# Performance work log

Hardware: AMD Instinct MI355X
Metric: run time of the kernel (lower is better)

## Reference

```python
import jax, jax.numpy as jnp
import numpy as np

B, N, D, H = 16, 576, 768, 8
HD = D // H
SCALE = HD ** -0.5
EPS = 1e-5  # torch LayerNorm default


def _ln(x, g, b):
    mu = jnp.mean(x, axis=-1, keepdims=True)
    var = jnp.mean(jnp.square(x - mu), axis=-1, keepdims=True)
    return (x - mu) * jax.lax.rsqrt(var + EPS) * g + b


def setup_inputs() -> dict:
    key = jax.random.key(0)
    ks = jax.random.split(key, 20)
    s = D ** -0.5
    inp = {
        "x1": jax.random.normal(ks[0], (B, N, D), jnp.float32),
        "x2": jax.random.normal(ks[1], (B, N, D), jnp.float32),
        # projection weights stored [in, out]
        "Wq": jax.random.normal(ks[2], (D, D), jnp.float32) * s,
        "bq": jnp.zeros((D,), jnp.float32),
        "Wk": jax.random.normal(ks[3], (D, D), jnp.float32) * s,
        "bk": jnp.zeros((D,), jnp.float32),
        "Wv": jax.random.normal(ks[4], (D, D), jnp.float32) * s,
        "bv": jnp.zeros((D,), jnp.float32),
        "Wo": jax.random.normal(ks[5], (D, D), jnp.float32) * s,
        "bo": jnp.zeros((D,), jnp.float32),
        "g1": jnp.ones((D,), jnp.float32),
        "be1": jnp.zeros((D,), jnp.float32),
        "g2": jnp.ones((D,), jnp.float32),
        "be2": jnp.zeros((D,), jnp.float32),
        "W1": jax.random.normal(ks[6], (D, 4 * D), jnp.float32) * s,
        "bf1": jnp.zeros((4 * D,), jnp.float32),
        "W2": jax.random.normal(ks[7], (4 * D, D), jnp.float32) * (4 * D) ** -0.5,
        "bf2": jnp.zeros((D,), jnp.float32),
    }
    return inp


def reference(x1, x2, Wq, bq, Wk, bk, Wv, bv, Wo, bo, g1, be1, g2, be2, W1, bf1, W2, bf2):
    def heads(x, W, b):
        # [B,N,D] -> [B,H,N,HD]
        return (x @ W + b).reshape(B, N, H, HD).transpose(0, 2, 1, 3)

    def block(xq, xkv):
        q = heads(xq, Wq, bq)
        k = heads(xkv, Wk, bk)
        v = heads(xkv, Wv, bv)
        attn = jax.nn.softmax(jnp.einsum('bhqd,bhkd->bhqk', q, k) * SCALE, axis=-1)
        o = jnp.einsum('bhqk,bhkd->bqhd', attn, v).reshape(B, N, D)
        o = o @ Wo + bo
        h = _ln(xq + o, g1, be1)
        f = jax.nn.gelu(h @ W1 + bf1, approximate=False) @ W2 + bf2
        return _ln(h + f, g2, be2), attn

    out1, a1 = block(x1, x2)
    out2, a2 = block(x2, x1)
    attn_map = (a1 + a2.transpose(0, 1, 3, 2)) * 0.5
    return out1, out2, attn_map
```

## Files before the change

### kernel.cpp

```cpp
#include <hip/hip_runtime.h>
#include <cstdint>
#include <cstddef>

#define B_   16
#define N_   576
#define D_   768
#define H_   8
#define HD_  96
#define DF_  3072
#define R_   (B_*N_)
#define SCALE_F 0.10206207261596575f

typedef __bf16 bf16;
typedef __attribute__((ext_vector_type(8))) __bf16 bf16x8;
typedef __attribute__((ext_vector_type(4))) __bf16 bf16x4;
typedef __attribute__((ext_vector_type(4))) float  f32x4;

__device__ __forceinline__ void gld_lds16(const void* g, void* l) {
  __builtin_amdgcn_global_load_lds((const __attribute__((address_space(1))) void*)g,
                                   (__attribute__((address_space(3))) void*)l,
                                   16, 0, 0);
}
__device__ __forceinline__ void nt_f32(float* p, float v) { __builtin_nontemporal_store(v, p); }
__device__ __forceinline__ float gelu_f(float v) {
  float u = 0.7978845608028654f * v * (1.0f + 0.044715f*v*v);
  float e = __expf(2.0f*u);
  float th = 1.0f - 2.0f/(e + 1.0f);
  return 0.5f*v*(1.0f + th);
}

__global__ void cast_f32_bf16_k(const float* __restrict__ x, bf16* __restrict__ y, int n4) {
  int i = blockIdx.x*256 + threadIdx.x;
  if (i >= n4) return;
  f32x4 v = ((const f32x4*)x)[i];
  union { bf16 h[4]; unsigned long long q; } u;
  u.h[0] = (bf16)v[0]; u.h[1] = (bf16)v[1]; u.h[2] = (bf16)v[2]; u.h[3] = (bf16)v[3];
  ((unsigned long long*)y)[i] = u.q;
}

__global__ void transpose_cast_k(const float* __restrict__ W, bf16* __restrict__ WT,
                                 int rows, int cols) {
  __shared__ float tile[32][33];
  int cb = blockIdx.x*32, rb = blockIdx.y*32;
  int tx = threadIdx.x, ty = threadIdx.y;
  #pragma unroll
  for (int i=0;i<32;i+=8)
    tile[ty+i][tx] = W[(size_t)(rb+ty+i)*cols + cb+tx];
  __syncthreads();
  #pragma unroll
  for (int i=0;i<32;i+=8)
    WT[(size_t)(cb+ty+i)*rows + rb+tx] = (bf16)tile[tx][ty+i];
}

__global__ void concat_bias_k(const float* a, const float* b, const float* c, float* o) {
  int i = blockIdx.x*256 + threadIdx.x;
  if (i < 768) o[i] = a[i];
  else if (i < 1536) o[i] = b[i-768];
  else if (i < 2304) o[i] = c[i-1536];
}

template<int EPI, int SWZ>
__global__ __launch_bounds__(512, 2) void gemm256_k(
    const bf16* __restrict__ A, const bf16* __restrict__ Bt,
    const float* __restrict__ bias,
    bf16* __restrict__ outB, bf16* __restrict__ outK, bf16* __restrict__ outVT,
    int Nn, int K, int nct)
{
  __shared__ __align__(16) char lds[65536];
  const int t = threadIdx.x;
  const int lane = t & 63, w = t >> 6, g = lane >> 4, r = lane & 15;
  const int wr = w >> 2, wc = w & 3;

  const int cpx = gridDim.x >> 3;
  const int xcd = blockIdx.x & 7, loc = blockIdx.x >> 3;
  int rt, ct;
  if (SWZ) {
    const int nrt_x = cpx / nct;
    ct = loc / nrt_x;
    rt = xcd * nrt_x + (loc - ct*nrt_x);
  } else {
    const int wg = xcd*cpx + loc;
    rt = wg / nct; ct = wg - rt*nct;
  }
  const size_t a0 = (size_t)rt*256, b0 = (size_t)ct*256;

  f32x4 acc[8][4];
  #pragma unroll
  for (int m=0;m<8;++m)
    #pragma unroll
    for (int n=0;n<4;++n) acc[m][n] = (f32x4){0.f,0.f,0.f,0.f};

  const int rbase = ((t>>6)<<4) + (t&15);
  const int kbase = ((t>>4)&3)*8;
  const bf16* Ab = A  + (a0 + rbase)*(size_t)K + kbase;
  const bf16* Bb = Bt + (b0 + rbase)*(size_t)K + kbase;
  const size_t rstep = (size_t)128*K;
  char* Al = lds + t*16;
  char* Bl = lds + 32768 + t*16;

#define STAGE256(tt, cc) do { \
    const size_t ko_ = (size_t)(tt)*32; \
    gld_lds16(Ab + ko_,         Al + (cc)*16384); \
    gld_lds16(Ab + rstep + ko_, Al + (cc)*16384 + 8192); \
    gld_lds16(Bb + ko_,         Bl + (cc)*16384); \
    gld_lds16(Bb + rstep + ko_, Bl + (cc)*16384 + 8192); \
  } while (0)

  const int NT = K >> 5;
  STAGE256(0, 0);
  for (int tt = 0; tt < NT; ++tt) {
    const int c = tt & 1;
    if (tt + 1 < NT) {
      STAGE256(tt + 1, c ^ 1);
      asm volatile("s_waitcnt vmcnt(4)" ::: "memory");
    } else {
      asm volatile("s_waitcnt vmcnt(0)" ::: "memory");
    }
    __builtin_amdgcn_sched_barrier(0);
    __builtin_amdgcn_s_barrier();
    __builtin_amdgcn_sched_barrier(0);

    const char* Ard = lds + c*16384 + (wr<<13) + lane*16;
    const char* Brd = lds + 32768 + c*16384 + (wc<<12) + lane*16;
    bf16x8 bfr[4], af[4];
    #pragma unroll
    for (int n=0;n<4;++n) bfr[n] = *(const bf16x8*)(Brd + n*1024);
    #pragma unroll
    for (int m=0;m<4;++m) af[m]  = *(const bf16x8*)(Ard + m*1024);
    __builtin_amdgcn_s_setprio(1);
    #pragma unroll
    for (int m=0;m<4;++m)
      #pragma unroll
      for (int n=0;n<4;++n)
        acc[m][n] = __builtin_amdgcn_mfma_f32_16x16x32_bf16(af[m], bfr[n], acc[m][n], 0, 0, 0);
    __builtin_amdgcn_s_setprio(0);
    #pragma unroll
    for (int m=0;m<4;++m) af[m] = *(const bf16x8*)(Ard + (4+m)*1024);
    __builtin_amdgcn_s_setprio(1);
    #pragma unroll
    for (int m=0;m<4;++m)
      #pragma unroll
      for (int n=0;n<4;++n)
        acc[4+m][n] = __builtin_amdgcn_mfma_f32_16x16x32_bf16(af[m], bfr[n], acc[4+m][n], 0, 0, 0);
    __builtin_amdgcn_s_setprio(0);
    __builtin_amdgcn_sched_barrier(0);
    __builtin_amdgcn_s_barrier();
    __builtin_amdgcn_sched_barrier(0);
  }
#undef STAGE256

  const int rowb = rt*256;
  const int colb = ct*256;
  bf16* lds16p = (bf16*)lds;
  const int g4 = g*4;
  const bool vtile = (EPI == 4) && (ct >= 6);

  #pragma unroll
  for (int ph = 0; ph < 2; ++ph) {
    __builtin_amdgcn_s_barrier();
    #pragma unroll
    for (int n = 0; n < 4; ++n) {
      const int col = wc*64 + n*16 + r;
      const float bc = bias[colb + col];
      #pragma unroll
      for (int m = 0; m < 4; ++m) {
        #pragma unroll
        for (int j = 0; j < 4; ++j) {
          float v = acc[ph*4+m][n][j] + bc;
          if (EPI == 3) v = gelu_f(v);
          const int rowin = m*16 + g4 + j;
          if (vtile) {
            lds16p[col*128 + wr*64 + (rowin ^ ((col&7)<<3))] = (bf16)v;
          } else {
            const int rowL = wr*64 + rowin;
            const int chs = ((col>>3) ^ ((rowL>>2)&7));
            lds16p[rowL*256 + (chs<<3) + (col&7)] = (bf16)v;
          }
        }
      }
    }
    __builtin_amdgcn_s_barrier();
    if (vtile) {
      #pragma unroll
      for (int i = 0; i < 8; ++i) {
        const int cid = i*512 + t;
        const int col = cid >> 4, chunk = cid & 15, run = chunk >> 3, k = chunk & 7;
        bf16x8 val = *(const bf16x8*)&lds16p[col*128 + run*64 + ((k ^ (col&7))<<3)];
        const int rowg = rowb + run*128 + ph*64 + k*8;
        const int s  = rowg >= R_;
        const int rr = rowg - s*R_;
        const int bb = rr / N_, nn = rr - bb*N_;
        bf16* p = outVT + (size_t)s*R_*D_ + ((size_t)bb*D_ + (ct-6)*256 + col)*N_ + nn;
        *(bf16x8*)p = val;
      }
    } else {
      #pragma unroll
      for (int i = 0; i < 8; ++i) {
        const int cid = i*512 + t;
        const int rl = cid >> 5, ch = cid & 31;
        bf16x8 val = *(const bf16x8*)&lds16p[rl*256 + ((ch ^ ((rl>>2)&7))<<3)];
        const int rowg = rowb + (rl>>6)*128 + ph*64 + (rl&63);
        const int c0 = colb + ch*8;
        if (EPI == 0 || EPI == 3) {
          *(bf16x8*)(outB + (size_t)rowg*Nn + c0) = val;
        } else {
          const int s  = rowg >= R_;
          const int rr = rowg - s*R_;
          const int bb = rr / N_, nn = rr - bb*N_;
          const size_t so = (size_t)s*R_*D_;
          bf16* p;
          if (c0 < 768) {
            const int hh = c0/96, dd = c0 - hh*96;
            p = outB + so + ((size_t)(bb*H_+hh)*N_ + nn)*HD_ + dd;
          } else {
            const int c1 = c0 - 768;
            const int hh = c1/96, dd = c1 - hh*96;
            p = outK + so + ((size_t)(bb*H_+hh)*N_ + nn)*HD_ + dd;
          }
          *(bf16x8*)p = val;
        }
      }
    }
  }
}


__global__ __launch_bounds__(256, 2) void attn_stats_k(
    const bf16* __restrict__ Q, const bf16* __restrict__ Kb,
    const bf16* __restrict__ VT, bf16* __restrict__ obuf,
    float* __restrict__ mrow, float* __restrict__ rrow)
{
  __shared__ __align__(16) char plds[2*18432 + 512];
  float* smax = (float*)(plds + 36864);
  float* ssum = smax + 64;
  const int t = threadIdx.x, w = t>>6, lane = t&63, g = lane>>4, r = lane&15;
  const int wq = w>>1, wc = w&1;
  const int h = blockIdx.x & 7, ii = blockIdx.x >> 3;
  const int b = ii/18, qt = ii - b*18, bh = b*8 + h;
  const int q0 = qt*32 + wq*16, c0 = wc*288, row4 = g*4;

  f32x4 s[18];
  #pragma unroll
  for (int n=0;n<18;++n) s[n] = (f32x4){0.f,0.f,0.f,0.f};
  bf16x8 aq[3];
  const bf16* qrow = Q + ((size_t)(b*H_+h)*N_ + q0 + r)*HD_;
  #pragma unroll
  for (int kk=0;kk<3;++kk) aq[kk] = *(const bf16x8*)(qrow + kk*32 + g*8);
  const bf16* kbase = Kb + ((size_t)(b*H_+h)*N_ + c0 + r)*HD_ + g*8;
  #pragma unroll
  for (int n=0;n<18;++n) {
    const bf16* kr = kbase + (size_t)(n*16)*HD_;
    bf16x8 b0 = *(const bf16x8*)(kr);
    bf16x8 b1 = *(const bf16x8*)(kr + 32);
    bf16x8 b2 = *(const bf16x8*)(kr + 64);
    __builtin_amdgcn_s_setprio(1);
    s[n] = __builtin_amdgcn_mfma_f32_16x16x32_bf16(aq[0], b0, s[n], 0, 0, 0);
    s[n] = __builtin_amdgcn_mfma_f32_16x16x32_bf16(aq[1], b1, s[n], 0, 0, 0);
    s[n] = __builtin_amdgcn_mfma_f32_16x16x32_bf16(aq[2], b2, s[n], 0, 0, 0);
    __builtin_amdgcn_s_setprio(0);
  }

  float mx[4], sum[4], rinv[4];
  #pragma unroll
  for (int j=0;j<4;++j) {
    float m = -1e30f;
    #pragma unroll
    for (int n=0;n<18;++n) m = fmaxf(m, s[n][j]);
    #pragma unroll
    for (int d=1; d<16; d<<=1) m = fmaxf(m, __shfl_xor(m, d));
    mx[j] = m;
  }
  if ((lane&15)==0) {
    #pragma unroll
    for (int j=0;j<4;++j) smax[(wq*2+wc)*16 + row4+j] = mx[j];
  }
  __syncthreads();
  #pragma unroll
  for (int j=0;j<4;++j) {
    mx[j] = fmaxf(mx[j], smax[(wq*2+(wc^1))*16 + row4+j]);
    sum[j] = 0.f;
  }
  #pragma unroll
  for (int n=0;n<18;++n)
    #pragma unroll
    for (int j=0;j<4;++j) {
      float p = __expf((s[n][j] - mx[j]) * SCALE_F);
      s[n][j] = p; sum[j] += p;
    }
  #pragma unroll
  for (int j=0;j<4;++j) {
    #pragma unroll
    for (int d=1; d<16; d<<=1) sum[j] += __shfl_xor(sum[j], d);
  }
  if ((lane&15)==0) {
    #pragma unroll
    for (int j=0;j<4;++j) ssum[(wq*2+wc)*16 + row4+j] = sum[j];
  }
  __syncthreads();
  #pragma unroll
  for (int j=0;j<4;++j)
    rinv[j] = 1.0f / (sum[j] + ssum[(wq*2+(wc^1))*16 + row4+j]);

  if (wc==0 && (lane&15)==0) {
    const size_t sb = (size_t)bh*N_ + q0 + row4;
    #pragma unroll
    for (int j=0;j<4;++j) { mrow[sb+j] = mx[j]; rrow[sb+j] = rinv[j]; }
  }

  char* pw = plds + wq*18432;
  #pragma unroll
  for (int n=0;n<18;++n)
    #pragma unroll
    for (int j=0;j<4;++j) {
      int kc = c0 + n*16 + r, row = row4 + j;
      *(bf16*)(pw + ((kc>>3)<<8) + (row<<4) + ((kc&7)<<1)) = (bf16)(s[n][j]*rinv[j]);
    }
  __syncthreads();

  f32x4 oa[3];
  #pragma unroll
  for (int n=0;n<3;++n) oa[n] = (f32x4){0.f,0.f,0.f,0.f};
  const bf16* vtb = VT + ((size_t)b*D_ + h*HD_ + wc*48 + r)*N_ + g*8;
  for (int kt=0; kt<18; ++kt) {
    bf16x8 pa = *(const bf16x8*)(pw + kt*1024 + lane*16);
    bf16x8 v0 = *(const bf16x8*)(vtb + kt*32);
    bf16x8 v1 = *(const bf16x8*)(vtb + (size_t)16*N_ + kt*32);
    bf16x8 v2 = *(const bf16x8*)(vtb + (size_t)32*N_ + kt*32);
    __builtin_amdgcn_s_setprio(1);
    oa[0] = __builtin_amdgcn_mfma_f32_16x16x32_bf16(pa, v0, oa[0], 0, 0, 0);
    oa[1] = __builtin_amdgcn_mfma_f32_16x16x32_bf16(pa, v1, oa[1], 0, 0, 0);
    oa[2] = __builtin_amdgcn_mfma_f32_16x16x32_bf16(pa, v2, oa[2], 0, 0, 0);
    __builtin_amdgcn_s_setprio(0);
  }
  #pragma unroll
  for (int n=0;n<3;++n)
    #pragma unroll
    for (int j=0;j<4;++j)
      obuf[((size_t)b*N_ + q0+row4+j)*D_ + h*HD_ + wc*48 + n*16 + r] = (bf16)oa[n][j];
}

__global__ __launch_bounds__(256, 2) void attn_map_k(
    const bf16* __restrict__ Q1, const bf16* __restrict__ K2,
    const bf16* __restrict__ VT2, const bf16* __restrict__ K1,
    const bf16* __restrict__ Q2, const float* __restrict__ mrow,
    const float* __restrict__ rrow, float* __restrict__ attn_out,
    bf16* __restrict__ obuf)
{
  __shared__ __align__(16) char plds[2*18432 + 512];
  float* smax = (float*)(plds + 36864);
  float* ssum = smax + 64;
  const int t = threadIdx.x, w = t>>6, lane = t&63, g = lane>>4, r = lane&15;
  const int wq = w>>1, wc = w&1;
  const int h = blockIdx.x & 7, ii = blockIdx.x >> 3;
  const int b = ii/18, qt = ii - b*18, bh = b*8 + h;
  const int q0 = qt*32 + wq*16, c0 = wc*288, row4 = g*4;

  f32x4 s[18];
  #pragma unroll
  for (int n=0;n<18;++n) s[n] = (f32x4){0.f,0.f,0.f,0.f};
  bf16x8 aq[3];
  const bf16* qrow = Q1 + ((size_t)(b*H_+h)*N_ + q0 + r)*HD_;
  #pragma unroll
  for (int kk=0;kk<3;++kk) aq[kk] = *(const bf16x8*)(qrow + kk*32 + g*8);
  const bf16* kbase = K2 + ((size_t)(b*H_+h)*N_ + c0 + r)*HD_ + g*8;
  #pragma unroll
  for (int n=0;n<18;++n) {
    const bf16* kr = kbase + (size_t)(n*16)*HD_;
    bf16x8 b0 = *(const bf16x8*)(kr);
    bf16x8 b1 = *(const bf16x8*)(kr + 32);
    bf16x8 b2 = *(const bf16x8*)(kr + 64);
    __builtin_amdgcn_s_setprio(1);
    s[n] = __builtin_amdgcn_mfma_f32_16x16x32_bf16(aq[0], b0, s[n], 0, 0, 0);
    s[n] = __builtin_amdgcn_mfma_f32_16x16x32_bf16(aq[1], b1, s[n], 0, 0, 0);
    s[n] = __builtin_amdgcn_mfma_f32_16x16x32_bf16(aq[2], b2, s[n], 0, 0, 0);
    __builtin_amdgcn_s_setprio(0);
  }

  float mx[4], sum[4], rinv[4];
  #pragma unroll
  for (int j=0;j<4;++j) {
    float m = -1e30f;
    #pragma unroll
    for (int n=0;n<18;++n) m = fmaxf(m, s[n][j]);
    #pragma unroll
    for (int d=1; d<16; d<<=1) m = fmaxf(m, __shfl_xor(m, d));
    mx[j] = m;
  }
  if ((lane&15)==0) {
    #pragma unroll
    for (int j=0;j<4;++j) smax[(wq*2+wc)*16 + row4+j] = mx[j];
  }
  __syncthreads();
  #pragma unroll
  for (int j=0;j<4;++j) {
    mx[j] = fmaxf(mx[j], smax[(wq*2+(wc^1))*16 + row4+j]);
    sum[j] = 0.f;
  }
  #pragma unroll
  for (int n=0;n<18;++n)
    #pragma unroll
    for (int j=0;j<4;++j) {
      float p = __expf((s[n][j] - mx[j]) * SCALE_F);
      s[n][j] = p; sum[j] += p;
    }
  #pragma unroll
  for (int j=0;j<4;++j) {
    #pragma unroll
    for (int d=1; d<16; d<<=1) sum[j] += __shfl_xor(sum[j], d);
  }
  if ((lane&15)==0) {
    #pragma unroll
    for (int j=0;j<4;++j) ssum[(wq*2+wc)*16 + row4+j] = sum[j];
  }
  __syncthreads();
  #pragma unroll
  for (int j=0;j<4;++j)
    rinv[j] = 1.0f / (sum[j] + ssum[(wq*2+(wc^1))*16 + row4+j]);

  char* pw = plds + wq*18432;
  #pragma unroll
  for (int n=0;n<18;++n)
    #pragma unroll
    for (int j=0;j<4;++j) {
      int kc = c0 + n*16 + r, row = row4 + j;
      *(bf16*)(pw + ((kc>>3)<<8) + (row<<4) + ((kc&7)<<1)) = (bf16)(s[n][j]*rinv[j]);
    }
  __syncthreads();

  f32x4 oa[3];
  #pragma unroll
  for (int n=0;n<3;++n) oa[n] = (f32x4){0.f,0.f,0.f,0.f};
  const bf16* vtb = VT2 + ((size_t)b*D_ + h*HD_ + wc*48 + r)*N_ + g*8;
  for (int kt=0; kt<18; ++kt) {
    bf16x8 pa = *(const bf16x8*)(pw + kt*1024 + lane*16);
    bf16x8 v0 = *(const bf16x8*)(vtb + kt*32);
    bf16x8 v1 = *(const bf16x8*)(vtb + (size_t)16*N_ + kt*32);
    bf16x8 v2 = *(const bf16x8*)(vtb + (size_t)32*N_ + kt*32);
    __builtin_amdgcn_s_setprio(1);
    oa[0] = __builtin_amdgcn_mfma_f32_16x16x32_bf16(pa, v0, oa[0], 0, 0, 0);
    oa[1] = __builtin_amdgcn_mfma_f32_16x16x32_bf16(pa, v1, oa[1], 0, 0, 0);
    oa[2] = __builtin_amdgcn_mfma_f32_16x16x32_bf16(pa, v2, oa[2], 0, 0, 0);
    __builtin_amdgcn_s_setprio(0);
  }
  #pragma unroll
  for (int n=0;n<3;++n)
    #pragma unroll
    for (int j=0;j<4;++j)
      obuf[((size_t)b*N_ + q0+row4+j)*D_ + h*HD_ + wc*48 + n*16 + r] = (bf16)oa[n][j];

  #pragma unroll
  for (int n=0;n<18;++n) s[n] = (f32x4){0.f,0.f,0.f,0.f};
  bf16x8 ak[3];
  const bf16* k1row = K1 + ((size_t)(b*H_+h)*N_ + q0 + r)*HD_;
  #pragma unroll
  for (int kk=0;kk<3;++kk) ak[kk] = *(const bf16x8*)(k1row + kk*32 + g*8);
  const bf16* q2b = Q2 + ((size_t)(b*H_+h)*N_ + c0 + r)*HD_ + g*8;
  #pragma unroll
  for (int n=0;n<18;++n) {
    const bf16* qr2 = q2b + (size_t)(n*16)*HD_;
    bf16x8 b0 = *(const bf16x8*)(qr2);
    bf16x8 b1 = *(const bf16x8*)(qr2 + 32);
    bf16x8 b2 = *(const bf16x8*)(qr2 + 64);
    __builtin_amdgcn_s_setprio(1);
    s[n] = __builtin_amdgcn_mfma_f32_16x16x32_bf16(ak[0], b0, s[n], 0, 0, 0);
    s[n] = __builtin_amdgcn_mfma_f32_16x16x32_bf16(ak[1], b1, s[n], 0, 0, 0);
    s[n] = __builtin_amdgcn_mfma_f32_16x16x32_bf16(ak[2], b2, s[n], 0, 0, 0);
    __builtin_amdgcn_s_setprio(0);
  }

  const float* mb = mrow + (size_t)bh*N_;
  const float* rb = rrow + (size_t)bh*N_;
  float* aout = attn_out + (size_t)bh*N_*N_;
  #pragma unroll
  for (int n=0;n<18;++n) {
    const int kc = c0 + n*16 + r;
    const float m2v = mb[kc];
    const float rv  = rb[kc];
    #pragma unroll
    for (int j=0;j<4;++j) {
      const int row = row4 + j;
      float p1 = (float)(*(const bf16*)(pw + ((kc>>3)<<8) + (row<<4) + ((kc&7)<<1)));
      float a2t = __expf((s[n][j] - m2v) * SCALE_F) * rv;
      nt_f32(aout + (size_t)(q0 + row)*N_ + kc, 0.5f*(p1 + a2t));
    }
  }
}

template<int MODE>
__global__ __launch_bounds__(256) void ln_k(
    const float* __restrict__ xf1, const float* __restrict__ xf2,
    const bf16* __restrict__ xb, const bf16* __restrict__ y,
    const float* __restrict__ gamma, const float* __restrict__ beta,
    bf16* __restrict__ out16, float* __restrict__ out32)
{
  const int w = threadIdx.x>>6, lane = threadIdx.x&63;
  const size_t row = (size_t)blockIdx.x*4 + w;
  float v[12]; float s = 0.f, s2 = 0.f;
  const bf16* yr = y + row*D_;
  #pragma unroll
  for (int i=0;i<3;++i) {
    int c = i*256 + lane*4;
    bf16x4 bb = *(const bf16x4*)(yr + c);
    float xr4[4];
    if (MODE == 0) {
      const float* xr = (row < R_) ? (xf1 + row*D_) : (xf2 + (row-R_)*D_);
      f32x4 a = *(const f32x4*)(xr + c);
      #pragma unroll
      for (int q=0;q<4;++q) xr4[q] = a[q];
    } else {
      bf16x4 a = *(const bf16x4*)(xb + row*D_ + c);
      #pragma unroll
      for (int q=0;q<4;++q) xr4[q] = (float)a[q];
    }
    #pragma unroll
    for (int q=0;q<4;++q) {
      float tq = xr4[q] + (float)bb[q];
      v[i*4+q] = tq; s += tq; s2 += tq*tq;
    }
  }
  #pragma unroll
  for (int d=1; d<64; d<<=1) { s += __shfl_xor(s, d); s2 += __shfl_xor(s2, d); }
  const float mean = s*(1.f/D_);
  const float var  = s2*(1.f/D_) - mean*mean;
  const float rstd = rsqrtf(var + 1e-5f);
  #pragma unroll
  for (int i=0;i<3;++i) {
    int c = i*256 + lane*4;
    f32x4 gm = *(const f32x4*)(gamma + c);
    f32x4 bt = *(const f32x4*)(beta  + c);
    float o[4];
    #pragma unroll
    for (int q=0;q<4;++q) o[q] = (v[i*4+q]-mean)*rstd*gm[q] + bt[q];
    if (MODE == 0) {
      union { bf16 h[4]; unsigned long long q64; } u;
      u.h[0]=(bf16)o[0]; u.h[1]=(bf16)o[1]; u.h[2]=(bf16)o[2]; u.h[3]=(bf16)o[3];
      *(unsigned long long*)(out16 + row*D_ + c) = u.q64;
    } else {
      f32x4 ov = {o[0], o[1], o[2], o[3]};
      __builtin_nontemporal_store(ov, (f32x4*)(out32 + row*D_ + c));
    }
  }
}

extern "C" void kernel_launch(void* const* d_in, const int* in_sizes, int n_in,
                              void* d_out, int out_size, void* d_ws, size_t ws_size,
                              hipStream_t stream)
{
  const float* x1  = (const float*)d_in[0];
  const float* x2  = (const float*)d_in[1];
  const float* Wq  = (const float*)d_in[2];  const float* bq  = (const float*)d_in[3];
  const float* Wk  = (const float*)d_in[4];  const float* bk  = (const float*)d_in[5];
  const float* Wv  = (const float*)d_in[6];  const float* bv  = (const float*)d_in[7];
  const float* Wo  = (const float*)d_in[8];  const float* bo  = (const float*)d_in[9];
  const float* g1  = (const float*)d_in[10]; const float* be1 = (const float*)d_in[11];
  const float* g2  = (const float*)d_in[12]; const float* be2 = (const float*)d_in[13];
  const float* W1  = (const float*)d_in[14]; const float* bf1 = (const float*)d_in[15];
  const float* W2  = (const float*)d_in[16]; const float* bf2 = (const float*)d_in[17];

  float* outLN = (float*)d_out;
  float* attn  = outLN + (size_t)2*R_*D_;

  char* ws = (char*)d_ws;
  size_t off = 0;
  auto alloc = [&](size_t bytes) -> void* {
    void* p = ws + off;
    off += (bytes + 255) & ~(size_t)255;
    return p;
  };
  const size_t RD2 = (size_t)R_*D_*2;
  size_t span1 = off;
  bf16* xb  = (bf16*)alloc(2*RD2);
  bf16* Qb  = (bf16*)alloc(2*RD2);
  bf16* Kb  = (bf16*)alloc(2*RD2);
  bf16* VTb = (bf16*)alloc(2*RD2);
  bf16* G   = (bf16*)(ws + span1);
  bf16* wqkvT = (bf16*)alloc((size_t)2304*D_*2);
  float* bqkv = (float*)alloc(2304*4);
  bf16* woT   = (bf16*)alloc((size_t)D_*D_*2);
  bf16* w1T   = (bf16*)alloc((size_t)D_*DF_*2);
  bf16* w2T   = (bf16*)alloc((size_t)DF_*D_*2);
  bf16* obuf  = (bf16*)alloc(2*RD2);
  bf16* oprojB= (bf16*)alloc(2*RD2);
  bf16* h16   = (bf16*)alloc(2*RD2);
  bf16* f16   = (bf16*)alloc(2*RD2);
  float* m2r  = (float*)alloc((size_t)B_*H_*N_*4);
  float* r2r  = (float*)alloc((size_t)B_*H_*N_*4);
  (void)ws_size; (void)in_sizes; (void)n_in; (void)out_size;

  const int n4 = R_*D_/4;
  cast_f32_bf16_k<<<n4/256, 256, 0, stream>>>(x1, xb, n4);
  cast_f32_bf16_k<<<n4/256, 256, 0, stream>>>(x2, xb + (size_t)R_*D_, n4);

  dim3 tb(32,8);
  transpose_cast_k<<<dim3(24,24), tb, 0, stream>>>(Wq, wqkvT,             D_, D_);
  transpose_cast_k<<<dim3(24,24), tb, 0, stream>>>(Wk, wqkvT + 768*D_,    D_, D_);
  transpose_cast_k<<<dim3(24,24), tb, 0, stream>>>(Wv, wqkvT + 1536*D_,   D_, D_);
  transpose_cast_k<<<dim3(24,24), tb, 0, stream>>>(Wo, woT, D_, D_);
  transpose_cast_k<<<dim3(96,24), tb, 0, stream>>>(W1, w1T, D_, DF_);
  transpose_cast_k<<<dim3(24,96), tb, 0, stream>>>(W2, w2T, DF_, D_);
  concat_bias_k<<<9, 256, 0, stream>>>(bq, bk, bv, bqkv);

  gemm256_k<4,1><<<648, 512, 0, stream>>>(xb, wqkvT, bqkv, Qb, Kb, VTb, 2304, 768, 9);

  const size_t SD = (size_t)R_*D_;
  attn_stats_k<<<2304, 256, 0, stream>>>(Qb + SD, Kb, VTb, obuf + SD, m2r, r2r);
  attn_map_k  <<<2304, 256, 0, stream>>>(Qb, Kb + SD, VTb + SD, Kb, Qb + SD, m2r, r2r, attn, obuf);

  gemm256_k<0,1><<<216, 512, 0, stream>>>(obuf, woT, bo, oprojB, nullptr, nullptr, 768, 768, 3);
  ln_k<0><<<2*R_/4, 256, 0, stream>>>(x1, x2, nullptr, oprojB, g1, be1, h16, nullptr);
  gemm256_k<3,1><<<864, 512, 0, stream>>>(h16, w1T, bf1, G, nullptr, nullptr, 3072, 768, 12);
  gemm256_k<0,0><<<216, 512, 0, stream>>>(G, w2T, bf2, f16, nullptr, nullptr, 768, 3072, 3);
  ln_k<1><<<2*R_/4, 256, 0, stream>>>(nullptr, nullptr, h16, f16, g2, be2, nullptr, outLN);
}
```

Before: 728.9 us.

## Deepen GEMM LDS pipeline with 64-wide K tiles and interleaved staged loads

Restructures the 256x256 bf16 GEMM main loop to use 64-wide K tiles split into two 32-wide halves. The loop is double-buffered across 128KB of LDS. Global-to-LDS loads for the next A and B halves are spread between the four MFMA quarter-phases, each fenced by barriers, so memory traffic overlaps compute at finer granularity. The larger LDS footprint likely allows only one workgroup per CU, and the extra barriers add synchronization cost.

```diff
diff --git a/kernel.cpp b/kernel.cpp
--- a/kernel.cpp
+++ b/kernel.cpp
@@ -66,10 +66,11 @@
     bf16* __restrict__ outB, bf16* __restrict__ outK, bf16* __restrict__ outVT,
     int Nn, int K, int nct)
 {
-  __shared__ __align__(16) char lds[65536];
+  __shared__ __align__(16) char lds[131072];
   const int t = threadIdx.x;
   const int lane = t & 63, w = t >> 6, g = lane >> 4, r = lane & 15;
   const int wr = w >> 2, wc = w & 3;
+  const int lane16 = lane*16;
 
   const int cpx = gridDim.x >> 3;
   const int xcd = blockIdx.x & 7, loc = blockIdx.x >> 3;
@@ -90,64 +91,70 @@
     #pragma unroll
     for (int n=0;n<4;++n) acc[m][n] = (f32x4){0.f,0.f,0.f,0.f};
 
-  const int rbase = ((t>>6)<<4) + (t&15);
-  const int kbase = ((t>>4)&3)*8;
-  const bf16* Ab = A  + (a0 + rbase)*(size_t)K + kbase;
-  const bf16* Bb = Bt + (b0 + rbase)*(size_t)K + kbase;
-  const size_t rstep = (size_t)128*K;
-  char* Al = lds + t*16;
-  char* Bl = lds + 32768 + t*16;
-
-#define STAGE256(tt, cc) do { \
-    const size_t ko_ = (size_t)(tt)*32; \
-    gld_lds16(Ab + ko_,         Al + (cc)*16384); \
-    gld_lds16(Ab + rstep + ko_, Al + (cc)*16384 + 8192); \
-    gld_lds16(Bb + ko_,         Bl + (cc)*16384); \
-    gld_lds16(Bb + rstep + ko_, Bl + (cc)*16384 + 8192); \
-  } while (0)
-
-  const int NT = K >> 5;
-  STAGE256(0, 0);
-  for (int tt = 0; tt < NT; ++tt) {
-    const int c = tt & 1;
-    if (tt + 1 < NT) {
-      STAGE256(tt + 1, c ^ 1);
-      asm volatile("s_waitcnt vmcnt(4)" ::: "memory");
-    } else {
-      asm volatile("s_waitcnt vmcnt(0)" ::: "memory");
-    }
-    __builtin_amdgcn_sched_barrier(0);
-    __builtin_amdgcn_s_barrier();
-    __builtin_amdgcn_sched_barrier(0);
-
-    const char* Ard = lds + c*16384 + (wr<<13) + lane*16;
-    const char* Brd = lds + 32768 + c*16384 + (wc<<12) + lane*16;
-    bf16x8 bfr[4], af[4];
-    #pragma unroll
-    for (int n=0;n<4;++n) bfr[n] = *(const bf16x8*)(Brd + n*1024);
-    #pragma unroll
-    for (int m=0;m<4;++m) af[m]  = *(const bf16x8*)(Ard + m*1024);
-    __builtin_amdgcn_s_setprio(1);
-    #pragma unroll
-    for (int m=0;m<4;++m)
-      #pragma unroll
-      for (int n=0;n<4;++n)
-        acc[m][n] = __builtin_amdgcn_mfma_f32_16x16x32_bf16(af[m], bfr[n], acc[m][n], 0, 0, 0);
-    __builtin_amdgcn_s_setprio(0);
-    #pragma unroll
-    for (int m=0;m<4;++m) af[m] = *(const bf16x8*)(Ard + (4+m)*1024);
-    __builtin_amdgcn_s_setprio(1);
-    #pragma unroll
-    for (int m=0;m<4;++m)
-      #pragma unroll
-      for (int n=0;n<4;++n)
-        acc[4+m][n] = __builtin_amdgcn_mfma_f32_16x16x32_bf16(af[m], bfr[n], acc[4+m][n], 0, 0, 0);
-    __builtin_amdgcn_s_setprio(0);
-    __builtin_amdgcn_sched_barrier(0);
-    __builtin_amdgcn_s_barrier();
-    __builtin_amdgcn_sched_barrier(0);
-  }
-#undef STAGE256
+  const bf16* Asrc = A  + (a0 + w*16 + (lane&15))*(size_t)K + ((lane>>4)<<3);
+  const bf16* Bsrc = Bt + (b0 + w*16 + (lane&15))*(size_t)K + ((lane>>4)<<3);
+  char* dstA = lds + t*16;
+  char* dstB = lds + 65536 + t*16;
+  const size_t row128 = (size_t)128*K;
+  const int NT = K >> 6;
+
+#define SA_(k,h) do { const size_t so_ = (size_t)(k)*64 + (h)*32; \
+    const int db_ = (((k)&1)<<15) + ((h)<<14); \
+    gld_lds16(Asrc + so_,          dstA + db_); \
+    gld_lds16(Asrc + row128 + so_, dstA + db_ + 8192); } while(0)
+#define SB_(k,h) do { const size_t so_ = (size_t)(k)*64 + (h)*32; \
+    const int db_ = (((k)&1)<<15) + ((h)<<14); \
+    gld_lds16(Bsrc + so_,          dstB + db_); \
+    gld_lds16(Bsrc + row128 + so_, dstB + db_ + 8192); } while(0)
+#define BAR_ do { __builtin_amdgcn_sched_barrier(0); __builtin_amdgcn_s_barrier(); \
+                  __builtin_amdgcn_sched_barrier(0); } while(0)
+#define MFMA16_(mo) do { __builtin_amdgcn_s_setprio(1); \
+    _Pragma("unroll") for (int m_=0;m_<4;++m_) \
+      _Pragma("unroll") for (int n_=0;n_<4;++n_) \
+        acc[(mo)+m_][n_] = __builtin_amdgcn_mfma_f32_16x16x32_bf16(af[m_], bfr[n_], acc[(mo)+m_][n_], 0, 0, 0); \
+    __builtin_amdgcn_s_setprio(0); } while(0)
+
+#define TILE_(tt, c) do { \
+    const char* ABv = lds + (c)*32768 + (wr<<13) + lane16; \
+    const char* BBv = lds + 65536 + (c)*32768 + (wc<<12) + lane16; \
+    bf16x8 bfr[4], af[4]; \
+     \
+    _Pragma("unroll") for (int n_=0;n_<4;++n_) bfr[n_] = *(const bf16x8*)(BBv + n_*1024); \
+    _Pragma("unroll") for (int m_=0;m_<4;++m_) af[m_]  = *(const bf16x8*)(ABv + m_*1024); \
+    if ((tt)+1 < NT) SA_((tt)+1, 1); \
+    BAR_; MFMA16_(0); BAR_; \
+     \
+    _Pragma("unroll") for (int m_=0;m_<4;++m_) af[m_] = *(const bf16x8*)(ABv + 4096 + m_*1024); \
+    if ((tt)+1 < NT) SB_((tt)+1, 1); \
+    BAR_; MFMA16_(4); BAR_; \
+     \
+    _Pragma("unroll") for (int n_=0;n_<4;++n_) bfr[n_] = *(const bf16x8*)(BBv + 16384 + n_*1024); \
+    _Pragma("unroll") for (int m_=0;m_<4;++m_) af[m_]  = *(const bf16x8*)(ABv + 16384 + m_*1024); \
+    if ((tt)+2 < NT) SA_((tt)+2, 0); \
+    BAR_; MFMA16_(0); BAR_; \
+     \
+    _Pragma("unroll") for (int m_=0;m_<4;++m_) af[m_] = *(const bf16x8*)(ABv + 16384 + 4096 + m_*1024); \
+    if ((tt)+2 < NT) { SB_((tt)+2, 0); \
+      asm volatile("s_waitcnt vmcnt(4)" ::: "memory"); \
+    } else if ((tt)+1 < NT) { \
+      asm volatile("s_waitcnt vmcnt(0)" ::: "memory"); \
+    } \
+    BAR_; MFMA16_(4); BAR_; \
+  } while(0)
+
+  SA_(0,0); SB_(0,0); SA_(0,1); SB_(0,1); SA_(1,0); SB_(1,0);
+  asm volatile("s_waitcnt vmcnt(4)" ::: "memory");
+  BAR_;
+
+  for (int tt = 0; tt < NT; tt += 2) {
+    TILE_(tt, 0);
+    TILE_(tt+1, 1);
+  }
+#undef TILE_
+#undef MFMA16_
+#undef BAR_
+#undef SB_
+#undef SA_
 
   const int rowb = rt*256;
   const int colb = ct*256;
```

Measured after the change: 704.3 us. -3.4%, faster.
